# Kernel tuning notes

Hardware: AMD Instinct MI355X
Metric: run time of the kernel (lower is better)

## Reference

```python
import jax, jax.numpy as jnp
import numpy as np

DIM = 256
HEAD_DIM = 64          # v head dim
HEAD_DIM_QK = 32       # q/k head dim
NUM_HEADS = DIM // HEAD_DIM          # 4
QK_DIM = HEAD_DIM_QK * NUM_HEADS     # 128
EPS = 1e-6


def setup_inputs() -> dict:
    key = jax.random.key(0)
    k1, k2, k3, k4, k5 = jax.random.split(key, 5)
    B, H, W, D = 2, 48, 48, 48
    x = jax.random.normal(k1, (B, DIM, H, W, D), dtype=jnp.float32)
    Wq = jax.random.normal(k2, (QK_DIM, DIM), dtype=jnp.float32) * 0.02
    Wk = jax.random.normal(k3, (QK_DIM, DIM), dtype=jnp.float32) * 0.02
    Wv = jax.random.normal(k4, (DIM, 1, 3, 3, 3), dtype=jnp.float32) * 0.1  # depthwise kernel
    bv = jax.random.normal(k5, (DIM,), dtype=jnp.float32) * 0.01
    return {"x": x, "Wq": Wq, "Wk": Wk, "Wv": Wv, "bv": bv}


def reference(x, Wq, Wk, Wv, bv):
    B, C, H, W, D = x.shape
    N = H * W * D
    nh, dqk, dv = NUM_HEADS, HEAD_DIM_QK, HEAD_DIM

    # 1x1x1 convs == channel matmuls -> [B, nh, dqk, N]
    q = jnp.einsum('oc,bchwd->bohwd', Wq, x).reshape(B, nh, dqk, N)
    k = jnp.einsum('oc,bchwd->bohwd', Wk, x).reshape(B, nh, dqk, N)

    # depthwise 3x3x3 conv (groups = C), padding 1
    v = jax.lax.conv_general_dilated(
        x, Wv, window_strides=(1, 1, 1), padding=[(1, 1), (1, 1), (1, 1)],
        dimension_numbers=('NCDHW', 'OIDHW', 'NCDHW'), feature_group_count=C)
    v = (v + bv[None, :, None, None, None]).reshape(B, nh, dv, N)

    # softmax feature maps: q over per-head channel dim, k over spatial dim
    q = jax.nn.softmax(q, axis=2)
    k = jax.nn.softmax(k, axis=3)

    # linear attention: kv = k @ v^T  -> [B, nh, dqk, dv]
    kv = jnp.einsum('bhkn,bhvn->bhkv', k, v)
    ksum = k.sum(axis=3)                                   # [B, nh, dqk]

    num = jnp.einsum('bhkn,bhkv->bhvn', q, kv)             # [B, nh, dv, N]
    Z = jnp.einsum('bhkn,bhk->bhn', q, ksum)               # [B, nh, N]
    out = num / (Z[:, :, None, :] + EPS)
    return out.reshape(B, C, H, W, D)
```

## Files before the change

### kernel.cpp

```cpp
#include <hip/hip_runtime.h>
#include <hip/hip_bf16.h>

static constexpr int CH   = 256;
static constexpr int NHD  = 4;
static constexpr int DV   = 64;
static constexpr int SY = 48, SX = 48, SZ = 48;
static constexpr int NPEN = SY * SX;
static constexpr int NPOS = NPEN * SZ;
static constexpr int PF2  = 128 * 80;

typedef float f32x4 __attribute__((ext_vector_type(4)));
typedef short bf8   __attribute__((ext_vector_type(8)));
union U16x4 { uint4 u; bf8 h; };

__device__ __forceinline__ ushort f2bf(float f) {
  return __bfloat16_as_ushort(__float2bfloat16(f));
}
__device__ __forceinline__ uint pk2(float lo, float hi) {
  return ((uint)f2bf(hi) << 16) | (uint)f2bf(lo);
}

__global__ __launch_bounds__(256) void k_prep2(
    const float* __restrict__ Wq, const float* __restrict__ Wk,
    ushort* __restrict__ Wqk2)
{
  const int i = blockIdx.x * 256 + threadIdx.x;
  const int rp = i >> 8, c = i & 255;
  const int h = rp >> 6, s = (rp >> 5) & 1, j = rp & 31;
  const float v = s ? Wk[(h * 32 + j) * 256 + c] : Wq[(h * 32 + j) * 256 + c];
  Wqk2[i] = f2bf(v);
}

__global__ __launch_bounds__(192) void k_conv3(
    const float* __restrict__ x, const float* __restrict__ Wv,
    const float* __restrict__ bv, __hip_bfloat16* __restrict__ vbuf,
    int y0s, int ys, int nyc)
{
  __shared__ float ring[4 * 2550];

  const int t   = threadIdx.x;
  const int bid = blockIdx.x;
  const int yc  = bid % nyc;
  const int c   = (bid / nyc) & 255;
  const int b   = bid / (nyc * 256);
  const int yst = y0s + yc * 12;

  const int cu = __builtin_amdgcn_readfirstlane(c);
  const float* xc = x + (size_t)(b * CH + cu) * NPOS;
  float wreg[27];
#pragma unroll
  for (int j = 0; j < 27; ++j) wreg[j] = Wv[cu * 27 + j];
  const float bias = bv[cu];

  for (int i = t; i < 4 * 2550; i += 192) ring[i] = 0.f;

  const int k0 = t, k1 = t + 192, k2 = t + 384;
  const int o0 = (1 + k0 / 12) * 51 + 1 + (k0 % 12) * 4;
  const int o1 = (1 + k1 / 12) * 51 + 1 + (k1 % 12) * 4;
  const int o2 = (1 + k2 / 12) * 51 + 1 + (k2 % 12) * 4;

  float4 v0, v1, v2;

#define SISSUE(gy_)                                                           \
  {                                                                           \
    const int g_ = (gy_);                                                     \
    if ((unsigned)g_ < 48u) {                                                 \
      const float* rp_ = xc + (size_t)g_ * NPEN;                              \
      v0 = *(const float4*)(rp_ + k0 * 4);                                    \
      v1 = *(const float4*)(rp_ + k1 * 4);                                    \
      v2 = *(const float4*)(rp_ + k2 * 4);                                    \
    } else {                                                                  \
      v0 = (float4){0.f,0.f,0.f,0.f}; v1 = v0; v2 = v0;                       \
    }                                                                         \
  }

#define SWRITE(slot_)                                                         \
  {                                                                           \
    float* pl_ = ring + (slot_) * 2550;                                       \
    pl_[o0+0]=v0.x; pl_[o0+1]=v0.y; pl_[o0+2]=v0.z; pl_[o0+3]=v0.w;           \
    pl_[o1+0]=v1.x; pl_[o1+1]=v1.y; pl_[o1+2]=v1.z; pl_[o1+3]=v1.w;           \
    pl_[o2+0]=v2.x; pl_[o2+1]=v2.y; pl_[o2+2]=v2.z; pl_[o2+3]=v2.w;           \
  }

  __syncthreads();

  SISSUE(yst - 1) SWRITE(0)
  SISSUE(yst)     SWRITE(1)
  SISSUE(yst + 1) SWRITE(2)
  __syncthreads();

  const int xq = t >> 2;
  const int zb = (t & 3) * 12;

  float accA[12], accB[12], outv[12];
#pragma unroll
  for (int i = 0; i < 12; ++i) { accA[i] = bias; accB[i] = bias; }

#define FOLD3(slot_)                                                          \
  {                                                                           \
    const float* P_ = ring + (slot_) * 2550;                                  \
    _Pragma("unroll")                                                         \
    for (int dx = 0; dx < 3; ++dx) {                                          \
      const float* B_ = P_ + (xq + dx) * 51 + zb;                             \
      float col[14];                                                          \
      _Pragma("unroll")                                                       \
      for (int k = 0; k < 14; ++k) col[k] = B_[k];                            \
      _Pragma("unroll")                                                       \
      for (int dz = 0; dz < 3; ++dz) {                                        \
        const float w2_ = wreg[18 + dx * 3 + dz];                             \
        const float w1_ = wreg[9  + dx * 3 + dz];                             \
        const float w0_ = wreg[     dx * 3 + dz];                             \
        _Pragma("unroll")                                                     \
        for (int i = 0; i < 12; ++i) {                                        \
          outv[i] = fmaf(w2_, col[i + dz], outv[i]);                          \
          accA[i] = fmaf(w1_, col[i + dz], accA[i]);                          \
          accB[i] = fmaf(w0_, col[i + dz], accB[i]);                          \
        }                                                                     \
      }                                                                       \
    }                                                                         \
  }

  {
    const float* P_ = ring + 0 * 2550;
#pragma unroll
    for (int dx = 0; dx < 3; ++dx) {
      const float* B_ = P_ + (xq + dx) * 51 + zb;
      float col[14];
#pragma unroll
      for (int k = 0; k < 14; ++k) col[k] = B_[k];
#pragma unroll
      for (int dz = 0; dz < 3; ++dz) {
        const float w0_ = wreg[dx * 3 + dz];
#pragma unroll
        for (int i = 0; i < 12; ++i)
          accA[i] = fmaf(w0_, col[i + dz], accA[i]);
      }
    }
  }
  {
    const float* P_ = ring + 1 * 2550;
#pragma unroll
    for (int dx = 0; dx < 3; ++dx) {
      const float* B_ = P_ + (xq + dx) * 51 + zb;
      float col[14];
#pragma unroll
      for (int k = 0; k < 14; ++k) col[k] = B_[k];
#pragma unroll
      for (int dz = 0; dz < 3; ++dz) {
        const float w1_ = wreg[9 + dx * 3 + dz];
        const float w0_ = wreg[    dx * 3 + dz];
#pragma unroll
        for (int i = 0; i < 12; ++i) {
          accA[i] = fmaf(w1_, col[i + dz], accA[i]);
          accB[i] = fmaf(w0_, col[i + dz], accB[i]);
        }
      }
    }
  }

  for (int r = 0; r < 12; ++r) {
    if (r < 11) SISSUE(yst + r + 2)

#pragma unroll
    for (int i = 0; i < 12; ++i) {
      outv[i] = accA[i];
      accA[i] = accB[i];
      accB[i] = bias;
    }
    FOLD3((r + 2) & 3)

    {
      const size_t o = (size_t)(b * CH + cu) * ((size_t)ys * NPEN) +
                       (size_t)(yst - y0s + r) * NPEN + xq * SZ + zb;
      uint2 s0, s1, s2;
      s0.x = pk2(outv[0], outv[1]);  s0.y = pk2(outv[2],  outv[3]);
      s1.x = pk2(outv[4], outv[5]);  s1.y = pk2(outv[6],  outv[7]);
      s2.x = pk2(outv[8], outv[9]);  s2.y = pk2(outv[10], outv[11]);
      __hip_bfloat16* dst = vbuf + o;
      *(uint2*)(dst)     = s0;
      *(uint2*)(dst + 4) = s1;
      *(uint2*)(dst + 8) = s2;
    }

    if (r < 11) SWRITE((r + 3) & 3)
    __syncthreads();
  }
#undef FOLD3
#undef SISSUE
#undef SWRITE
}

__global__ __launch_bounds__(512) void k_fuse(
    const float* __restrict__ x, const ushort* __restrict__ Wqk2,
    const ushort* __restrict__ vbuf, uint* __restrict__ qsm,
    float* __restrict__ partials, int y0s, int ys, int first, int nbh)
{
  __shared__ float xf[2][CH * 64];
  __shared__ short scr[8 * 32 * 40];

  const int t    = threadIdx.x;
  const int lane = t & 63;
  const int w    = __builtin_amdgcn_readfirstlane(t >> 6);
  const int h    = w >> 1, nh = w & 1;
  const int l15  = lane & 15, lg = lane >> 4;
  const int bid  = blockIdx.x;
  const int b    = (bid >= nbh) ? 1 : 0;
  const int bh   = bid - b * nbh;
  const int ntiles = ys * 36;
  const size_t Nsl = (size_t)ys * NPEN;

  const float*  xb = x + (size_t)b * CH * NPOS + (size_t)y0s * NPEN;
  const ushort* vb = vbuf + (size_t)(b * CH + h * 64) * Nsl;
  short* myscr = &scr[w * 32 * 40];
  const int gn_base = y0s * NPEN + nh * 32 + l15;
  uint* qhead = qsm + (size_t)(b * 4 + h) * 16 * NPOS;

  bf8 Bones;
  {
    const short o = (l15 == 0) ? (short)0x3F80 : (short)0;
#pragma unroll
    for (int j = 0; j < 8; ++j) Bones[j] = o;
  }

  f32x4 C2[2][5];
#pragma unroll
  for (int i = 0; i < 2; ++i)
#pragma unroll
    for (int j = 0; j < 5; ++j) C2[i][j] = (f32x4){0.f, 0.f, 0.f, 0.f};

  const int nr0 = (nh * 32 + 0  + l15 + lg * 8) & 63;
  const int nr1 = (nh * 32 + 16 + l15 + lg * 8) & 63;

#define STAGE(tile_, buf_)                                                     \
  {                                                                            \
    const int n0_ = (tile_) * 64;                                              \
    _Pragma("unroll")                                                          \
    for (int j_ = 0; j_ < 8; ++j_) {                                           \
      const int k_  = j_ * 512 + t;                 \
      const int c_  = k_ >> 4;                                                 \
      const int ci_ = k_ & 15;                                                 \
      const int rot_ = ((c_ >> 3) & 3) << 1;       \
      const int nq_  = ((ci_ - rot_) & 15) << 2;                               \
      const float* src_ = xb + (size_t)c_ * NPOS + n0_ + nq_;                  \
      __builtin_amdgcn_global_load_lds(                                        \
          (const __attribute__((address_space(1))) void*)src_,                 \
          (__attribute__((address_space(3))) void*)((char*)xf +                \
              ((buf_) * 4096 + j_ * 512 + w * 64) * 16),                       \
          16, 0, 0);                                                           \
    }                                                                          \
  }

  int cur = 0;
  if (bh < ntiles) STAGE(bh, 0)

  for (int tile = bh; tile < ntiles; tile += nbh) {
    const int n0 = tile * 64;
    __syncthreads();

    if (tile + nbh < ntiles) STAGE(tile + nbh, cur ^ 1)

    uint4 vr[4];
#pragma unroll
    for (int ct = 0; ct < 4; ++ct)
      vr[ct] = *(const uint4*)&vb[(size_t)(ct * 16 + l15) * Nsl +
                                  n0 + nh * 32 + lg * 8];

    f32x4 C1[4][2];
#pragma unroll
    for (int rt = 0; rt < 4; ++rt)
#pragma unroll
      for (int ct = 0; ct < 2; ++ct) C1[rt][ct] = (f32x4){0.f, 0.f, 0.f, 0.f};

#pragma unroll
    for (int ks = 0; ks < 8; ++ks) {
      const int c0 = ks * 32 + lg * 8;
      U16x4 a[4];
#pragma unroll
      for (int rt = 0; rt < 4; ++rt)
        a[rt].u = *(const uint4*)&Wqk2[(size_t)(h * 64 + rt * 16 + l15) * 256 + c0];
      bf8 Bf[2];
      {
        float f0[8], f1[8];
#pragma unroll
        for (int j = 0; j < 8; ++j) {
          const float* row = &xf[cur][(c0 + j) * 64];
          f0[j] = row[nr0];
          f1[j] = row[nr1];
        }
#pragma unroll
        for (int j = 0; j < 8; ++j) {
          Bf[0][j] = (short)f2bf(f0[j]);
          Bf[1][j] = (short)f2bf(f1[j]);
        }
      }
#pragma unroll
      for (int rt = 0; rt < 4; ++rt)
#pragma unroll
        for (int ct = 0; ct < 2; ++ct)
          C1[rt][ct] = __builtin_amdgcn_mfma_f32_16x16x32_bf16(
              a[rt].h, Bf[ct], C1[rt][ct], 0, 0, 0);
    }

#pragma unroll
    for (int ct = 0; ct < 2; ++ct) {
      float m = -1e30f;
#pragma unroll
      for (int rt = 0; rt < 2; ++rt)
#pragma unroll
        for (int r = 0; r < 4; ++r) m = fmaxf(m, C1[rt][ct][r]);
      m = fmaxf(m, __shfl_xor(m, 16));
      m = fmaxf(m, __shfl_xor(m, 32));
      float e[2][4], s = 0.f;
#pragma unroll
      for (int rt = 0; rt < 2; ++rt)
#pragma unroll
        for (int r = 0; r < 4; ++r) { e[rt][r] = __expf(C1[rt][ct][r] - m); s += e[rt][r]; }
      s += __shfl_xor(s, 16);
      s += __shfl_xor(s, 32);
      const float inv = 1.f / s;
      uint* qn = qhead + gn_base + n0 + ct * 16;
#pragma unroll
      for (int rt = 0; rt < 2; ++rt) {
        const int j0 = rt * 8 + lg * 2;
        qn[(size_t)(j0 + 0) * NPOS] = pk2(e[rt][0] * inv, e[rt][1] * inv);
        qn[(size_t)(j0 + 1) * NPOS] = pk2(e[rt][2] * inv, e[rt][3] * inv);
      }
    }

#pragma unroll
    for (int rt2 = 0; rt2 < 2; ++rt2)
#pragma unroll
      for (int ct = 0; ct < 2; ++ct) {
        const int nl = ct * 16 + l15;
#pragma unroll
        for (int r = 0; r < 4; ++r)
          myscr[(rt2 * 16 + lg * 4 + r) * 40 + nl] =
              (short)f2bf(__expf(C1[rt2 + 2][ct][r]));
      }

    __asm__ __volatile__("" ::: "memory");
    bf8 A2[2];
#pragma unroll
    for (int rt2 = 0; rt2 < 2; ++rt2)
      A2[rt2] = *(const bf8*)&myscr[(rt2 * 16 + l15) * 40 + lg * 8];
#pragma unroll
    for (int rt2 = 0; rt2 < 2; ++rt2) {
#pragma unroll
      for (int ct = 0; ct < 4; ++ct) {
        U16x4 v_; v_.u = vr[ct];
        C2[rt2][ct] = __builtin_amdgcn_mfma_f32_16x16x32_bf16(
            A2[rt2], v_.h, C2[rt2][ct], 0, 0, 0);
      }
      C2[rt2][4] = __builtin_amdgcn_mfma_f32_16x16x32_bf16(
          A2[rt2], Bones, C2[rt2][4], 0, 0, 0);
    }

    cur ^= 1;
  }
#undef STAGE

  __syncthreads();
  float* comb = (float*)xf;
  if (nh == 1) {
    float* dst = comb + (h * 64 + lane) * 40;
#pragma unroll
    for (int rt2 = 0; rt2 < 2; ++rt2)
#pragma unroll
      for (int ct = 0; ct < 5; ++ct)
#pragma unroll
        for (int r = 0; r < 4; ++r)
          dst[rt2 * 20 + ct * 4 + r] = C2[rt2][ct][r];
  }
  __syncthreads();
  if (nh == 0) {
    const float* srcp = comb + (h * 64 + lane) * 40;
    float* pb = partials + (size_t)bid * PF2;
#pragma unroll
    for (int rt2 = 0; rt2 < 2; ++rt2)
#pragma unroll
      for (int ct = 0; ct < 5; ++ct)
#pragma unroll
        for (int r = 0; r < 4; ++r) {
          const float v2 = C2[rt2][ct][r] + srcp[rt2 * 20 + ct * 4 + r];
          const int row = h * 32 + rt2 * 16 + lg * 4 + r;
          const int col = ct * 16 + l15;
          const int idx = row * 80 + col;
          if (first) pb[idx] = v2;
          else       pb[idx] += v2;
        }
  }
}

__global__ __launch_bounds__(256) void k_red_a(
    const float* __restrict__ partials, float* __restrict__ partial2, int nbh)
{
  const int bid = blockIdx.x;
  const int ec  = bid % 40, kc = (bid / 40) & 7, b = bid / 320;
  const int e   = ec * 256 + threadIdx.x;
  if (e >= PF2) return;
  const int kpc = nbh / 8;
  const float* pbase = partials + (size_t)(b * nbh + kc * kpc) * PF2 + e;
  float s0 = 0.f, s1 = 0.f, s2 = 0.f, s3 = 0.f;
  for (int k = 0; k < kpc; k += 4) {
    s0 += pbase[(size_t)(k + 0) * PF2];
    s1 += pbase[(size_t)(k + 1) * PF2];
    s2 += pbase[(size_t)(k + 2) * PF2];
    s3 += pbase[(size_t)(k + 3) * PF2];
  }
  partial2[(size_t)(b * 8 + kc) * PF2 + e] = (s0 + s1) + (s2 + s3);
}

__global__ __launch_bounds__(256) void k_red_s(
    const float* __restrict__ partial2, float* __restrict__ Sfin)
{
  const int t = threadIdx.x;
  const int b = t >> 7, kc = t & 127;
  float s = 0.f;
#pragma unroll
  for (int j = 0; j < 8; ++j)
    s += partial2[(size_t)(b * 8 + j) * PF2 + kc * 80 + 64];
  Sfin[b * 128 + kc] = s;
}

__global__ __launch_bounds__(256) void k_red_b(
    const float* __restrict__ partial2, const float* __restrict__ Sfin,
    float* __restrict__ kvn)
{
  const int bid = blockIdx.x;
  const int chunk = bid & 31, b = bid >> 5;
  const int e = chunk * 256 + threadIdx.x;
  const int kc = e >> 6, dv = e & 63;
  float s = 0.f;
#pragma unroll
  for (int j = 0; j < 8; ++j)
    s += partial2[(size_t)(b * 8 + j) * PF2 + kc * 80 + dv];
  kvn[(size_t)b * 8192 + e] = s / (Sfin[b * 128 + kc] * (1.f + 1e-6f));
}

__global__ __launch_bounds__(256) void k_out2(
    const uint* __restrict__ qsm, const float* __restrict__ kvn,
    float* __restrict__ out)
{
  const int t = threadIdx.x, lane = t & 63;
  const int w = __builtin_amdgcn_readfirstlane(t >> 6);
  const int bid = blockIdx.x;
  const int b  = bid / 1728;
  const int n0 = (bid % 1728) * 64;

  const uint* qp = qsm + (size_t)(b * 4 + w) * 16 * NPOS + n0 + lane;
  uint q[16];
#pragma unroll
  for (int j = 0; j < 16; ++j) q[j] = qp[(size_t)j * NPOS];
  float qa[32];
#pragma unroll
  for (int j = 0; j < 16; ++j) {
    qa[2 * j]     = __uint_as_float(q[j] << 16);
    qa[2 * j + 1] = __uint_as_float(q[j] & 0xFFFF0000u);
  }

  float oa[64];
#pragma unroll
  for (int d = 0; d < 64; ++d) oa[d] = 0.f;
  const float* kvh = kvn + (size_t)b * 8192 + (size_t)(w * 32) * 64;
#pragma unroll
  for (int kc = 0; kc < 32; ++kc) {
    const float* kr = kvh + kc * 64;
#pragma unroll
    for (int d = 0; d < 64; ++d) oa[d] = fmaf(qa[kc], kr[d], oa[d]);
  }
  float* ob = out + (size_t)(b * CH + w * DV) * NPOS + n0 + lane;
#pragma unroll
  for (int d = 0; d < 64; ++d) ob[(size_t)d * NPOS] = oa[d];
}

extern "C" void kernel_launch(void* const* d_in, const int* in_sizes, int n_in,
                              void* d_out, int out_size, void* d_ws, size_t ws_size,
                              hipStream_t stream)
{
  const float* x  = (const float*)d_in[0];
  const float* Wq = (const float*)d_in[1];
  const float* Wk = (const float*)d_in[2];
  const float* Wv = (const float*)d_in[3];
  const float* bv = (const float*)d_in[4];
  float* out = (float*)d_out;
  float* ws  = (float*)d_ws;

  ushort* Wqk2    = (ushort*)ws;
  uint*   qsm     = (uint*)(ws + 32768);
  float*  kvn     = ws + 32768 + 14155776;
  float*  Sfin    = kvn + 16384;
  float*  partial2= Sfin + 256;
  const size_t fixed0 = 32768 + 14155776 + 16384 + 256 + (size_t)16 * PF2;
  float*  partials = partial2 + 16 * PF2;

  const size_t wsf = ws_size / 4;
  static const int cand[][2] = {
    {128,48},{128,24},{64,24},{128,12},{64,12},{32,12}};
  int nbh = 32, ys = 12;
  for (int i = 0; i < 6; ++i) {
    const size_t need = fixed0 + (size_t)(2 * cand[i][0]) * PF2
                      + (size_t)cand[i][1] * 589824;
    if (need <= wsf) { nbh = cand[i][0]; ys = cand[i][1]; break; }
  }
  __hip_bfloat16* vbuf = (__hip_bfloat16*)(partials + (size_t)(2 * nbh) * PF2);

  k_prep2<<<256, 256, 0, stream>>>(Wq, Wk, Wqk2);

  const int nslab = 48 / ys;
  const int nyc = ys / 12;
  for (int s = 0; s < nslab; ++s) {
    k_conv3<<<2 * 256 * nyc, 192, 0, stream>>>(x, Wv, bv, vbuf, s * ys, ys, nyc);
    k_fuse <<<2 * nbh,       512, 0, stream>>>(x, Wqk2, (const ushort*)vbuf, qsm,
                                               partials, s * ys, ys,
                                               (s == 0) ? 1 : 0, nbh);
  }
  k_red_a<<<640, 256, 0, stream>>>(partials, partial2, nbh);
  k_red_s<<<1,   256, 0, stream>>>(partial2, Sfin);
  k_red_b<<<64,  256, 0, stream>>>(partial2, Sfin, kvn);
  k_out2 <<<2 * 1728, 256, 0, stream>>>(qsm, kvn, out);
}
```

Before: 293.2 us.

## Give each wave a private halo slab in depthwise conv to drop block barriers

```diff
diff --git a/kernel.cpp b/kernel.cpp
--- a/kernel.cpp
+++ b/kernel.cpp
@@ -36,14 +36,17 @@
     const float* __restrict__ bv, __hip_bfloat16* __restrict__ vbuf,
     int y0s, int ys, int nyc)
 {
-  __shared__ float ring[4 * 2550];
-
-  const int t   = threadIdx.x;
-  const int bid = blockIdx.x;
-  const int yc  = bid % nyc;
-  const int c   = (bid / nyc) & 255;
-  const int b   = bid / (nyc * 256);
-  const int yst = y0s + yc * 12;
+  __shared__ float ring[3][2][18 * 51];
+
+  const int t    = threadIdx.x;
+  const int lane = t & 63;
+  const int w    = __builtin_amdgcn_readfirstlane(t >> 6);
+  const int bid  = blockIdx.x;
+  const int yc   = bid % nyc;
+  const int c    = (bid / nyc) & 255;
+  const int b    = bid / (nyc * 256);
+  const int yst  = y0s + yc * 12;
+  const int x0   = w * 16;
 
   const int cu = __builtin_amdgcn_readfirstlane(c);
   const float* xc = x + (size_t)(b * CH + cu) * NPOS;
@@ -52,56 +55,67 @@
   for (int j = 0; j < 27; ++j) wreg[j] = Wv[cu * 27 + j];
   const float bias = bv[cu];
 
-  for (int i = t; i < 4 * 2550; i += 192) ring[i] = 0.f;
-
-  const int k0 = t, k1 = t + 192, k2 = t + 384;
-  const int o0 = (1 + k0 / 12) * 51 + 1 + (k0 % 12) * 4;
-  const int o1 = (1 + k1 / 12) * 51 + 1 + (k1 % 12) * 4;
-  const int o2 = (1 + k2 / 12) * 51 + 1 + (k2 % 12) * 4;
-
-  float4 v0, v1, v2;
+  float* my0 = &ring[w][0][0];
+  float* my1 = &ring[w][1][0];
+  for (int i = lane; i < 2 * 18 * 51; i += 64) my0[i] = 0.f;
+
+  const int cid0 = lane, cid1 = lane + 64, cid2 = lane + 128, cid3 = lane + 192;
+  const bool has3 = (lane < 24);
+  const int co0 = (cid0 / 12) * 51 + 1 + (cid0 % 12) * 4;
+  const int co1 = (cid1 / 12) * 51 + 1 + (cid1 % 12) * 4;
+  const int co2 = (cid2 / 12) * 51 + 1 + (cid2 % 12) * 4;
+  const int co3 = ((has3 ? cid3 : 192) / 12) * 51 + 1 + ((has3 ? cid3 : 192) % 12) * 4;
+  int  go0, go1, go2, go3;
+  bool gv0, gv1, gv2, gv3;
+  {
+    const int g0 = x0 - 1 + cid0 / 12, g1 = x0 - 1 + cid1 / 12;
+    const int g2 = x0 - 1 + cid2 / 12, g3 = x0 - 1 + cid3 / 12;
+    gv0 = (unsigned)g0 < 48u; gv1 = (unsigned)g1 < 48u;
+    gv2 = (unsigned)g2 < 48u; gv3 = has3 && ((unsigned)g3 < 48u);
+    go0 = g0 * SZ + (cid0 % 12) * 4;  go1 = g1 * SZ + (cid1 % 12) * 4;
+    go2 = g2 * SZ + (cid2 % 12) * 4;  go3 = g3 * SZ + (cid3 % 12) * 4;
+  }
+
+  float4 v0, v1, v2, v3;
 
 #define SISSUE(gy_)                                                           \
   {                                                                           \
     const int g_ = (gy_);                                                     \
     if ((unsigned)g_ < 48u) {                                                 \
       const float* rp_ = xc + (size_t)g_ * NPEN;                              \
-      v0 = *(const float4*)(rp_ + k0 * 4);                                    \
-      v1 = *(const float4*)(rp_ + k1 * 4);                                    \
-      v2 = *(const float4*)(rp_ + k2 * 4);                                    \
+      v0 = gv0 ? *(const float4*)(rp_ + go0) : (float4){0.f,0.f,0.f,0.f};     \
+      v1 = gv1 ? *(const float4*)(rp_ + go1) : (float4){0.f,0.f,0.f,0.f};     \
+      v2 = gv2 ? *(const float4*)(rp_ + go2) : (float4){0.f,0.f,0.f,0.f};     \
+      v3 = gv3 ? *(const float4*)(rp_ + go3) : (float4){0.f,0.f,0.f,0.f};     \
     } else {                                                                  \
-      v0 = (float4){0.f,0.f,0.f,0.f}; v1 = v0; v2 = v0;                       \
+      v0 = (float4){0.f,0.f,0.f,0.f}; v1 = v0; v2 = v0; v3 = v0;              \
     }                                                                         \
   }
 
-#define SWRITE(slot_)                                                         \
+#define SWRITE(PL_)                                                           \
   {                                                                           \
-    float* pl_ = ring + (slot_) * 2550;                                       \
-    pl_[o0+0]=v0.x; pl_[o0+1]=v0.y; pl_[o0+2]=v0.z; pl_[o0+3]=v0.w;           \
-    pl_[o1+0]=v1.x; pl_[o1+1]=v1.y; pl_[o1+2]=v1.z; pl_[o1+3]=v1.w;           \
-    pl_[o2+0]=v2.x; pl_[o2+1]=v2.y; pl_[o2+2]=v2.z; pl_[o2+3]=v2.w;           \
-  }
-
-  __syncthreads();
-
-  SISSUE(yst - 1) SWRITE(0)
-  SISSUE(yst)     SWRITE(1)
-  SISSUE(yst + 1) SWRITE(2)
-  __syncthreads();
-
-  const int xq = t >> 2;
-  const int zb = (t & 3) * 12;
-
-  float accA[12], accB[12], outv[12];
-#pragma unroll
-  for (int i = 0; i < 12; ++i) { accA[i] = bias; accB[i] = bias; }
-
-#define FOLD3(slot_)                                                          \
+    float* pl_ = (PL_);                                                       \
+    pl_[co0+0]=v0.x; pl_[co0+1]=v0.y; pl_[co0+2]=v0.z; pl_[co0+3]=v0.w;       \
+    pl_[co1+0]=v1.x; pl_[co1+1]=v1.y; pl_[co1+2]=v1.z; pl_[co1+3]=v1.w;       \
+    pl_[co2+0]=v2.x; pl_[co2+1]=v2.y; pl_[co2+2]=v2.z; pl_[co2+3]=v2.w;       \
+    if (has3) {                                                               \
+      pl_[co3+0]=v3.x; pl_[co3+1]=v3.y; pl_[co3+2]=v3.z; pl_[co3+3]=v3.w;     \
+    }                                                                         \
+  }
+
+  const int xl = lane >> 2;
+  const int zb = (lane & 3) * 12;
+
+  float accP[12], accQ[12], accN[12];
+#pragma unroll
+  for (int i = 0; i < 12; ++i) { accP[i] = bias; accQ[i] = bias; }
+
+#define FOLD3(PL_)                                                            \
   {                                                                           \
-    const float* P_ = ring + (slot_) * 2550;                                  \
+    const float* P_ = (PL_);                                                  \
     _Pragma("unroll")                                                         \
     for (int dx = 0; dx < 3; ++dx) {                                          \
-      const float* B_ = P_ + (xq + dx) * 51 + zb;                             \
+      const float* B_ = P_ + (xl + dx) * 51 + zb;                             \
       float col[14];                                                          \
       _Pragma("unroll")                                                       \
       for (int k = 0; k < 14; ++k) col[k] = B_[k];                            \
@@ -112,19 +126,47 @@
         const float w0_ = wreg[     dx * 3 + dz];                             \
         _Pragma("unroll")                                                     \
         for (int i = 0; i < 12; ++i) {                                        \
-          outv[i] = fmaf(w2_, col[i + dz], outv[i]);                          \
-          accA[i] = fmaf(w1_, col[i + dz], accA[i]);                          \
-          accB[i] = fmaf(w0_, col[i + dz], accB[i]);                          \
+          accP[i] = fmaf(w2_, col[i + dz], accP[i]);                          \
+          accQ[i] = fmaf(w1_, col[i + dz], accQ[i]);                          \
+          accN[i] = fmaf(w0_, col[i + dz], accN[i]);                          \
         }                                                                     \
       }                                                                       \
     }                                                                         \
   }
 
+#define STORE(r_)                                                             \
+  {                                                                           \
+    const size_t o_ = (size_t)(b * CH + cu) * ((size_t)ys * NPEN) +           \
+                      (size_t)(yst - y0s + (r_)) * NPEN + (x0 + xl) * SZ + zb;\
+    uint2 s0_, s1_, s2_;                                                      \
+    s0_.x = pk2(accP[0], accP[1]);  s0_.y = pk2(accP[2],  accP[3]);           \
+    s1_.x = pk2(accP[4], accP[5]);  s1_.y = pk2(accP[6],  accP[7]);           \
+    s2_.x = pk2(accP[8], accP[9]);  s2_.y = pk2(accP[10], accP[11]);          \
+    __hip_bfloat16* dst_ = vbuf + o_;                                         \
+    *(uint2*)(dst_)     = s0_;                                                \
+    *(uint2*)(dst_ + 4) = s1_;                                                \
+    *(uint2*)(dst_ + 8) = s2_;                                                \
+  }
+
+#define ROWPHASE(r_, PF_, PW_)                                                \
+  {                                                                           \
+    if ((r_) < 11) SISSUE(yst + (r_) + 2)                                     \
+    _Pragma("unroll")                                                         \
+    for (int i = 0; i < 12; ++i) accN[i] = bias;                              \
+    FOLD3(PF_)                                                 \
+    STORE(r_)                                                                 \
+    _Pragma("unroll")                                                         \
+    for (int i = 0; i < 12; ++i) { accP[i] = accQ[i]; accQ[i] = accN[i]; }    \
+    if ((r_) < 11) SWRITE(PW_)                                 \
+  }
+
+  SISSUE(yst - 1) SWRITE(my0)
+  SISSUE(yst)
   {
-    const float* P_ = ring + 0 * 2550;
+    const float* P_ = my0;
 #pragma unroll
     for (int dx = 0; dx < 3; ++dx) {
-      const float* B_ = P_ + (xq + dx) * 51 + zb;
+      const float* B_ = P_ + (xl + dx) * 51 + zb;
       float col[14];
 #pragma unroll
       for (int k = 0; k < 14; ++k) col[k] = B_[k];
@@ -133,15 +175,17 @@
         const float w0_ = wreg[dx * 3 + dz];
 #pragma unroll
         for (int i = 0; i < 12; ++i)
-          accA[i] = fmaf(w0_, col[i + dz], accA[i]);
+          accP[i] = fmaf(w0_, col[i + dz], accP[i]);
       }
     }
   }
+  SWRITE(my1)
+  SISSUE(yst + 1)
   {
-    const float* P_ = ring + 1 * 2550;
+    const float* P_ = my1;
 #pragma unroll
     for (int dx = 0; dx < 3; ++dx) {
-      const float* B_ = P_ + (xq + dx) * 51 + zb;
+      const float* B_ = P_ + (xl + dx) * 51 + zb;
       float col[14];
 #pragma unroll
       for (int k = 0; k < 14; ++k) col[k] = B_[k];
@@ -151,40 +195,21 @@
         const float w0_ = wreg[    dx * 3 + dz];
 #pragma unroll
         for (int i = 0; i < 12; ++i) {
-          accA[i] = fmaf(w1_, col[i + dz], accA[i]);
-          accB[i] = fmaf(w0_, col[i + dz], accB[i]);
+          accP[i] = fmaf(w1_, col[i + dz], accP[i]);
+          accQ[i] = fmaf(w0_, col[i + dz], accQ[i]);
         }
       }
     }
   }
-
-  for (int r = 0; r < 12; ++r) {
-    if (r < 11) SISSUE(yst + r + 2)
-
-#pragma unroll
-    for (int i = 0; i < 12; ++i) {
-      outv[i] = accA[i];
-      accA[i] = accB[i];
-      accB[i] = bias;
-    }
-    FOLD3((r + 2) & 3)
-
-    {
-      const size_t o = (size_t)(b * CH + cu) * ((size_t)ys * NPEN) +
-                       (size_t)(yst - y0s + r) * NPEN + xq * SZ + zb;
-      uint2 s0, s1, s2;
-      s0.x = pk2(outv[0], outv[1]);  s0.y = pk2(outv[2],  outv[3]);
-      s1.x = pk2(outv[4], outv[5]);  s1.y = pk2(outv[6],  outv[7]);
-      s2.x = pk2(outv[8], outv[9]);  s2.y = pk2(outv[10], outv[11]);
-      __hip_bfloat16* dst = vbuf + o;
-      *(uint2*)(dst)     = s0;
-      *(uint2*)(dst + 4) = s1;
-      *(uint2*)(dst + 8) = s2;
-    }
-
-    if (r < 11) SWRITE((r + 3) & 3)
-    __syncthreads();
-  }
+  SWRITE(my0)
+
+#pragma unroll
+  for (int g = 0; g < 6; ++g) {
+    ROWPHASE(g * 2 + 0, my0, my1)
+    ROWPHASE(g * 2 + 1, my1, my0)
+  }
+#undef ROWPHASE
+#undef STORE
 #undef FOLD3
 #undef SISSUE
 #undef SWRITE
```

Result: slower. 318.4 us (+8.6%).
